# Optimization experiments

Measured on AMD Instinct MI355X. Metric: run time of the kernel, lower is better.

## Reference

```python
import jax, jax.numpy as jnp
import numpy as np

N = 50000     # nodes
E = 800000    # edges (avg degree 16)
DIN = 128     # in_size
DH = 256      # hidden_size
P = 100000    # pos/neg edge pairs


def _w(key, fan_in, shape):
    return jax.random.normal(key, shape, jnp.float32) * (1.0 / np.sqrt(fan_in))


def setup_inputs() -> dict:
    key = jax.random.key(0)
    ks = jax.random.split(key, 24)
    inp = {}
    inp['x'] = jax.random.normal(ks[0], (N, DIN), jnp.float32)
    inp['edge_src'] = jax.random.randint(ks[1], (E,), 0, N, dtype=jnp.int32)
    inp['edge_dst'] = jax.random.randint(ks[2], (E,), 0, N, dtype=jnp.int32)
    inp['pos_src'] = jax.random.randint(ks[3], (P,), 0, N, dtype=jnp.int32)
    inp['pos_dst'] = jax.random.randint(ks[4], (P,), 0, N, dtype=jnp.int32)
    inp['neg_src'] = jax.random.randint(ks[5], (P,), 0, N, dtype=jnp.int32)
    inp['neg_dst'] = jax.random.randint(ks[6], (P,), 0, N, dtype=jnp.int32)
    # SAGEConv layers: fc_self + fc_neigh + bias
    dims = [(DIN, DH), (DH, DH), (DH, DH)]
    for i, (di, do) in enumerate(dims):
        inp[f'Ws{i}'] = _w(ks[7 + 3 * i], di, (di, do))
        inp[f'Wn{i}'] = _w(ks[8 + 3 * i], di, (di, do))
        inp[f'b{i}'] = jnp.zeros((do,), jnp.float32)
    # predictor MLP: DH -> DH -> DH -> 1
    inp['Wp1'] = _w(ks[16], DH, (DH, DH)); inp['bp1'] = jnp.zeros((DH,), jnp.float32)
    inp['Wp2'] = _w(ks[17], DH, (DH, DH)); inp['bp2'] = jnp.zeros((DH,), jnp.float32)
    inp['Wp3'] = _w(ks[18], DH, (DH, 1)); inp['bp3'] = jnp.zeros((1,), jnp.float32)
    return inp


def _sage_layer(h, src, dst, Ws, Wn, b):
    # mean aggregation over incoming edges, then fc_self(h) + fc_neigh(agg) + b
    n = h.shape[0]
    msg = h[src]                                              # [E, d] gather
    deg = jax.ops.segment_sum(jnp.ones((src.shape[0],), h.dtype), dst, num_segments=n)
    agg = jax.ops.segment_sum(msg, dst, num_segments=n)
    agg = agg / jnp.maximum(deg, 1.0)[:, None]
    return h @ Ws + agg @ Wn + b


def reference(x, edge_src, edge_dst, pos_src, pos_dst, neg_src, neg_dst,
              Ws0, Wn0, b0, Ws1, Wn1, b1, Ws2, Wn2, b2,
              Wp1, bp1, Wp2, bp2, Wp3, bp3):
    h = x
    layers = [(Ws0, Wn0, b0), (Ws1, Wn1, b1), (Ws2, Wn2, b2)]
    for i, (Ws, Wn, bb) in enumerate(layers):
        h = _sage_layer(h, edge_src, edge_dst, Ws, Wn, bb)
        if i < len(layers) - 1:
            h = jax.nn.relu(h)

    def predictor(e):
        z = jax.nn.relu(e @ Wp1 + bp1)
        z = jax.nn.relu(z @ Wp2 + bp2)
        return z @ Wp3 + bp3

    hidden_pos = predictor(h[pos_src] * h[pos_dst])   # [P, 1]
    hidden_neg = predictor(h[neg_src] * h[neg_dst])   # [P, 1]
    return (hidden_pos, hidden_neg)
```

## Files before the change

### kernel.cpp

```cpp
#include <hip/hip_runtime.h>
#include <hip/hip_bf16.h>

#define CDIV(a, b) (((a) + (b) - 1) / (b))

typedef __attribute__((ext_vector_type(8))) __bf16 bf16x8;
typedef __attribute__((ext_vector_type(2))) __bf16 bf16x2;
typedef __attribute__((ext_vector_type(4))) float f32x4;

__device__ __forceinline__ float bf2f(unsigned short u) {
  union { unsigned int i; float f; } c; c.i = ((unsigned int)u) << 16; return c.f;
}
__device__ __forceinline__ unsigned short f2bf(float f) {
  union { float f; unsigned int i; } c; c.f = f;
  unsigned int r = c.i + 0x7fffu + ((c.i >> 16) & 1u);
  return (unsigned short)(r >> 16);
}
__device__ __forceinline__ unsigned int cvt2(float a, float b) {
  bf16x2 v; v[0] = (__bf16)a; v[1] = (__bf16)b;
  union { bf16x2 v; unsigned int u; } c; c.v = v; return c.u;
}
__device__ __forceinline__ unsigned short cvt1(float a) {
  __bf16 b = (__bf16)a;
  union { __bf16 b; unsigned short u; } c; c.b = b; return c.u;
}

__global__ void k_detect(const unsigned short* __restrict__ xq, int nsamp, int* __restrict__ flagp) {
  __shared__ float sm[256];
  int t = threadIdx.x;
  float mx = 0.f;
  for (int i = t; i < nsamp; i += 256) {
    float v = bf2f(xq[i]);
    if (!(v == v)) v = 1e30f;
    mx = fmaxf(mx, fabsf(v));
  }
  sm[t] = mx; __syncthreads();
  for (int o = 128; o > 0; o >>= 1) {
    if (t < o) sm[t] = fmaxf(sm[t], sm[t + o]);
    __syncthreads();
  }
  if (t == 0) *flagp = (sm[0] > 1e6f) ? 1 : 0;
}

__global__ void k_cvt7(const void* p0, const void* p1, const void* p2, const void* p3,
                       const void* p4, const void* p5, const void* p6,
                       float* d0, float* d1, float* d2, float* d3,
                       float* d4, float* d5, float* d6, const int* __restrict__ flagp) {
  int b = blockIdx.x, t = threadIdx.x;
  const void* s = 0; float* d = 0; int n = 256;
  switch (b) {
    case 0: s = p0; d = d0; break;
    case 1: s = p1; d = d1; break;
    case 2: s = p2; d = d2; break;
    case 3: s = p3; d = d3; break;
    case 4: s = p4; d = d4; break;
    case 5: s = p5; d = d5; break;
    default: s = p6; d = d6; n = 1; break;
  }
  if (t < n) d[t] = (*flagp) ? ((const float*)s)[t] : bf2f(((const unsigned short*)s)[t]);
}

__global__ void k_wh(const void* __restrict__ W, unsigned short* __restrict__ Bth,
                     int K, const int* __restrict__ flagp) {
  int i = blockIdx.x * 256 + threadIdx.x;
  if (i >= K * 256) return;
  int k = i >> 8, n = i & 255;
  float v = (*flagp) ? ((const float*)W)[i] : bf2f(((const unsigned short*)W)[i]);
  Bth[(size_t)n * K + k] = f2bf(v);
}

__global__ void k_xbf16(const void* __restrict__ x, unsigned short* __restrict__ Xb, int n,
                        const int* __restrict__ flagp) {
  int i = blockIdx.x * 256 + threadIdx.x;
  if (i >= n) return;
  float v = (*flagp) ? ((const float*)x)[i] : bf2f(((const unsigned short*)x)[i]);
  Xb[i] = f2bf(v);
}

__global__ void k_zero_i32(int* p, int n) {
  int i = blockIdx.x * 256 + threadIdx.x;
  if (i < n) p[i] = 0;
}

__global__ void k_deg(const int* __restrict__ dst, int* __restrict__ deg, int E) {
  int e = blockIdx.x * 256 + threadIdx.x;
  if (e < E) atomicAdd(&deg[dst[e]], 1);
}
__global__ void k_scan1(const int* __restrict__ in, int* __restrict__ out, int* __restrict__ bsums, int n) {
  __shared__ int sh[256];
  int t = threadIdx.x, i = blockIdx.x * 256 + t;
  int v = (i < n) ? in[i] : 0;
  sh[t] = v; __syncthreads();
  for (int o = 1; o < 256; o <<= 1) {
    int add = (t >= o) ? sh[t - o] : 0;
    __syncthreads();
    sh[t] += add;
    __syncthreads();
  }
  if (i < n) out[i] = sh[t] - v;
  if (t == 255) bsums[blockIdx.x] = sh[255];
}
__global__ void k_scan2(int* bsums, int nb) {
  __shared__ int sh[256];
  int t = threadIdx.x;
  int v = (t < nb) ? bsums[t] : 0;
  sh[t] = v; __syncthreads();
  for (int o = 1; o < 256; o <<= 1) {
    int add = (t >= o) ? sh[t - o] : 0;
    __syncthreads();
    sh[t] += add;
    __syncthreads();
  }
  if (t < nb) bsums[t] = sh[t] - v;
}
__global__ void k_scan3(int* offs, const int* bsums, int n, int etot) {
  int i = blockIdx.x * 256 + threadIdx.x;
  if (i < n) offs[i] += bsums[blockIdx.x];
  if (i == 0) offs[n] = etot;
}
__global__ void k_copy_i32(const int* __restrict__ a, int* __restrict__ b, int n) {
  int i = blockIdx.x * 256 + threadIdx.x;
  if (i < n) b[i] = a[i];
}
__global__ void k_fill(const int* __restrict__ dst, const int* __restrict__ src,
                       int* __restrict__ cursor, int* __restrict__ csr_src, int E) {
  int e = blockIdx.x * 256 + threadIdx.x;
  if (e >= E) return;
  int pos = atomicAdd(&cursor[dst[e]], 1);
  csr_src[pos] = src[e];
}
__global__ void k_sortw(const int* __restrict__ offs, int* __restrict__ csr, int n) {
  int w = threadIdx.x >> 6, lane = threadIdx.x & 63;
  int v = blockIdx.x * 4 + w;
  if (v >= n) return;
  int s = offs[v], e = offs[v + 1];
  int deg = e - s;
  if (deg <= 1) return;
  if (deg > 64) {
    if (lane == 0) {
      for (int i = s + 1; i < e; ++i) {
        int key = csr[i], j = i - 1;
        while (j >= s && csr[j] > key) { csr[j + 1] = csr[j]; --j; }
        csr[j + 1] = key;
      }
    }
    return;
  }
  int val = (lane < deg) ? csr[s + lane] : 0x7fffffff;
#pragma unroll
  for (int k = 2; k <= 64; k <<= 1) {
    bool dir = (lane & k) == 0;
#pragma unroll
    for (int j = k >> 1; j > 0; j >>= 1) {
      int p = __shfl_xor(val, j, 64);
      bool lower = (lane & j) == 0;
      val = (lower == dir) ? min(val, p) : max(val, p);
    }
  }
  if (lane < deg) csr[s + lane] = val;
}

__global__ void k_agg(const unsigned short* __restrict__ H, int Kd,
                      const int* __restrict__ offs, const int* __restrict__ csr,
                      unsigned short* __restrict__ Ab) {
  int w = threadIdx.x >> 6, lane = threadIdx.x & 63;
  int v = blockIdx.x * 4 + w;
  int s = offs[v], e = offs[v + 1];
  float inv = 1.f / fmaxf((float)(e - s), 1.f);
  if (Kd == 256) {
    int c4 = lane * 4;
    float a0 = 0.f, a1 = 0.f, a2 = 0.f, a3 = 0.f;
    int i = s;
    for (; i + 4 <= e; i += 4) {
      uint2 z0 = *(const uint2*)&H[(size_t)csr[i] * 256 + c4];
      uint2 z1 = *(const uint2*)&H[(size_t)csr[i + 1] * 256 + c4];
      uint2 z2 = *(const uint2*)&H[(size_t)csr[i + 2] * 256 + c4];
      uint2 z3 = *(const uint2*)&H[(size_t)csr[i + 3] * 256 + c4];
      a0 += bf2f((unsigned short)z0.x) + bf2f((unsigned short)z1.x)
          + bf2f((unsigned short)z2.x) + bf2f((unsigned short)z3.x);
      a1 += bf2f((unsigned short)(z0.x >> 16)) + bf2f((unsigned short)(z1.x >> 16))
          + bf2f((unsigned short)(z2.x >> 16)) + bf2f((unsigned short)(z3.x >> 16));
      a2 += bf2f((unsigned short)z0.y) + bf2f((unsigned short)z1.y)
          + bf2f((unsigned short)z2.y) + bf2f((unsigned short)z3.y);
      a3 += bf2f((unsigned short)(z0.y >> 16)) + bf2f((unsigned short)(z1.y >> 16))
          + bf2f((unsigned short)(z2.y >> 16)) + bf2f((unsigned short)(z3.y >> 16));
    }
    for (; i < e; ++i) {
      uint2 z0 = *(const uint2*)&H[(size_t)csr[i] * 256 + c4];
      a0 += bf2f((unsigned short)z0.x);
      a1 += bf2f((unsigned short)(z0.x >> 16));
      a2 += bf2f((unsigned short)z0.y);
      a3 += bf2f((unsigned short)(z0.y >> 16));
    }
    uint2 o;
    o.x = cvt2(a0 * inv, a1 * inv);
    o.y = cvt2(a2 * inv, a3 * inv);
    *(uint2*)&Ab[(size_t)v * 256 + c4] = o;
  } else {
    int c2 = lane * 2;
    float a0 = 0.f, a1 = 0.f;
    int i = s;
    for (; i + 4 <= e; i += 4) {
      unsigned int z0 = *(const unsigned int*)&H[(size_t)csr[i] * 128 + c2];
      unsigned int z1 = *(const unsigned int*)&H[(size_t)csr[i + 1] * 128 + c2];
      unsigned int z2 = *(const unsigned int*)&H[(size_t)csr[i + 2] * 128 + c2];
      unsigned int z3 = *(const unsigned int*)&H[(size_t)csr[i + 3] * 128 + c2];
      a0 += bf2f((unsigned short)z0) + bf2f((unsigned short)z1)
          + bf2f((unsigned short)z2) + bf2f((unsigned short)z3);
      a1 += bf2f((unsigned short)(z0 >> 16)) + bf2f((unsigned short)(z1 >> 16))
          + bf2f((unsigned short)(z2 >> 16)) + bf2f((unsigned short)(z3 >> 16));
    }
    for (; i < e; ++i) {
      unsigned int z0 = *(const unsigned int*)&H[(size_t)csr[i] * 128 + c2];
      a0 += bf2f((unsigned short)z0);
      a1 += bf2f((unsigned short)(z0 >> 16));
    }
    *(unsigned int*)&Ab[(size_t)v * 128 + c2] = cvt2(a0 * inv, a1 * inv);
  }
}

__global__ __launch_bounds__(256) void gemm_cat(
    const unsigned short* __restrict__ A1, const unsigned short* __restrict__ A2, int K,
    const unsigned short* __restrict__ B1h, const unsigned short* __restrict__ B2h,
    const float* __restrict__ bias, int relu, int M, unsigned short* __restrict__ O) {
  __shared__ unsigned short sAh[128 * 40], sBh[128 * 40];
  int t = threadIdx.x;
  int mt = blockIdx.x >> 1, nt = blockIdx.x & 1;
  int m0 = mt * 128;
  int n0 = nt * 128;
  int wid = t >> 6, lane = t & 63;
  int wr = (wid >> 1) * 64, wc = (wid & 1) * 64;
  int quad = lane >> 4, lrow = lane & 15;

  f32x4 acc[4][4];
  const f32x4 z4 = {0.f, 0.f, 0.f, 0.f};
#pragma unroll
  for (int i = 0; i < 4; ++i)
#pragma unroll
    for (int j = 0; j < 4; ++j) acc[i][j] = z4;

  int sr = t >> 2;
  int c8 = (t & 3) * 8;
  int ar0 = m0 + sr;      if (ar0 >= M) ar0 = M - 1;
  int ar1 = m0 + sr + 64; if (ar1 >= M) ar1 = M - 1;
  int br0 = n0 + sr, br1 = n0 + sr + 64;

  int kc = K >> 5;
  int nsteps = kc * 2;

  uint4 pfA0 = *(const uint4*)&A1[(size_t)ar0 * K + c8];
  uint4 pfA1 = *(const uint4*)&A1[(size_t)ar1 * K + c8];
  uint4 pfB0 = *(const uint4*)&B1h[(size_t)br0 * K + c8];
  uint4 pfB1 = *(const uint4*)&B1h[(size_t)br1 * K + c8];

  for (int s2 = 0; s2 < nsteps; ++s2) {
    *(uint4*)&sAh[sr * 40 + c8] = pfA0;
    *(uint4*)&sAh[(sr + 64) * 40 + c8] = pfA1;
    *(uint4*)&sBh[sr * 40 + c8] = pfB0;
    *(uint4*)&sBh[(sr + 64) * 40 + c8] = pfB1;
    int s1 = s2 + 1;
    if (s1 < nsteps) {
      const unsigned short* Ap = (s1 >= kc) ? A2 : A1;
      const unsigned short* Bp = (s1 >= kc) ? B2h : B1h;
      int k0 = ((s1 >= kc) ? (s1 - kc) : s1) * 32;
      pfA0 = *(const uint4*)&Ap[(size_t)ar0 * K + k0 + c8];
      pfA1 = *(const uint4*)&Ap[(size_t)ar1 * K + k0 + c8];
      pfB0 = *(const uint4*)&Bp[(size_t)br0 * K + k0 + c8];
      pfB1 = *(const uint4*)&Bp[(size_t)br1 * K + k0 + c8];
    }
    __syncthreads();
    bf16x8 ah[4], bh[4];
#pragma unroll
    for (int i = 0; i < 4; ++i) {
      ah[i] = *(const bf16x8*)&sAh[(wr + i * 16 + lrow) * 40 + quad * 8];
      bh[i] = *(const bf16x8*)&sBh[(wc + i * 16 + lrow) * 40 + quad * 8];
    }
#pragma unroll
    for (int i = 0; i < 4; ++i)
#pragma unroll
      for (int j = 0; j < 4; ++j)
        acc[i][j] = __builtin_amdgcn_mfma_f32_16x16x32_bf16(ah[i], bh[j], acc[i][j], 0, 0, 0);
    __syncthreads();
  }

#pragma unroll
  for (int j = 0; j < 4; ++j) {
    int gc = n0 + wc + j * 16 + lrow;
    float bv = bias[gc];
#pragma unroll
    for (int i = 0; i < 4; ++i) {
#pragma unroll
      for (int rr = 0; rr < 4; ++rr) {
        int gr = m0 + wr + i * 16 + quad * 4 + rr;
        if (gr < M) {
          float v = acc[i][j][rr] + bv;
          if (relu) v = fmaxf(v, 0.f);
          O[(size_t)gr * 256 + gc] = cvt1(v);
        }
      }
    }
  }
}

__global__ __launch_bounds__(256, 3) void gemm_pred_fused(
    const unsigned short* __restrict__ Hb,
    const int* __restrict__ ps, const int* __restrict__ pd,
    const int* __restrict__ ns, const int* __restrict__ nd,
    int nPos,
    const unsigned short* __restrict__ B1h, const float* __restrict__ bp1c,
    const unsigned short* __restrict__ B2h, const float* __restrict__ bp2c,
    const float* __restrict__ wp3, const float* __restrict__ bp3c,
    void* __restrict__ out, const int* __restrict__ flagp) {
  __shared__ __align__(16) unsigned short zT[64 * 264];
  __shared__ __align__(16) unsigned short sBh[256 * 40];
  int t = threadIdx.x;
  int m0 = blockIdx.x * 64;
  int wid = t >> 6, lane = t & 63;
  int wc = wid * 64;
  int quad = lane >> 4, lrow = lane & 15;

  int sr = t >> 2;
  int c8 = (t & 3) * 8;
  int c64 = (t & 3) * 64;

  int arow = m0 + sr;
  int s, d;
  if (arow < nPos) { s = ps[arow]; d = pd[arow]; }
  else             { s = ns[arow - nPos]; d = nd[arow - nPos]; }
  const unsigned short* Hs = &Hb[(size_t)s * 256];
  const unsigned short* Hd = &Hb[(size_t)d * 256];

#pragma unroll
  for (int u = 0; u < 8; ++u) {
    uint4 hs = *(const uint4*)(Hs + c64 + u * 8);
    uint4 hd = *(const uint4*)(Hd + c64 + u * 8);
    uint4 o;
    o.x = cvt2(bf2f((unsigned short)hs.x) * bf2f((unsigned short)hd.x),
               bf2f((unsigned short)(hs.x >> 16)) * bf2f((unsigned short)(hd.x >> 16)));
    o.y = cvt2(bf2f((unsigned short)hs.y) * bf2f((unsigned short)hd.y),
               bf2f((unsigned short)(hs.y >> 16)) * bf2f((unsigned short)(hd.y >> 16)));
    o.z = cvt2(bf2f((unsigned short)hs.z) * bf2f((unsigned short)hd.z),
               bf2f((unsigned short)(hs.z >> 16)) * bf2f((unsigned short)(hd.z >> 16)));
    o.w = cvt2(bf2f((unsigned short)hs.w) * bf2f((unsigned short)hd.w),
               bf2f((unsigned short)(hs.w >> 16)) * bf2f((unsigned short)(hd.w >> 16)));
    *(uint4*)&zT[sr * 264 + c64 + u * 8] = o;
  }

  f32x4 acc[4][4];
  const f32x4 z4 = {0.f, 0.f, 0.f, 0.f};
#pragma unroll
  for (int i = 0; i < 4; ++i)
#pragma unroll
    for (int j = 0; j < 4; ++j) acc[i][j] = z4;

  for (int k0 = 0; k0 < 256; k0 += 32) {
#pragma unroll
    for (int rep = 0; rep < 4; ++rep) {
      int r = sr + rep * 64;
      *(uint4*)&sBh[r * 40 + c8] = *(const uint4*)&B1h[(size_t)r * 256 + k0 + c8];
    }
    __syncthreads();
    bf16x8 ah[4], bh[4];
#pragma unroll
    for (int i = 0; i < 4; ++i) {
      ah[i] = *(const bf16x8*)&zT[(i * 16 + lrow) * 264 + k0 + quad * 8];
      bh[i] = *(const bf16x8*)&sBh[(wc + i * 16 + lrow) * 40 + quad * 8];
    }
    __builtin_amdgcn_s_setprio(1);
#pragma unroll
    for (int i = 0; i < 4; ++i)
#pragma unroll
      for (int j = 0; j < 4; ++j)
        acc[i][j] = __builtin_amdgcn_mfma_f32_16x16x32_bf16(ah[i], bh[j], acc[i][j], 0, 0, 0);
    __builtin_amdgcn_s_setprio(0);
    __syncthreads();
  }

#pragma unroll
  for (int j = 0; j < 4; ++j) {
    int gc = wc + j * 16 + lrow;
    float bv = bp1c[gc];
#pragma unroll
    for (int i = 0; i < 4; ++i) {
#pragma unroll
      for (int rr = 0; rr < 4; ++rr) {
        int rloc = i * 16 + quad * 4 + rr;
        float v = fmaxf(acc[i][j][rr] + bv, 0.f);
        zT[rloc * 264 + gc] = cvt1(v);
      }
    }
  }

#pragma unroll
  for (int i = 0; i < 4; ++i)
#pragma unroll
    for (int j = 0; j < 4; ++j) acc[i][j] = z4;

  for (int k0 = 0; k0 < 256; k0 += 32) {
#pragma unroll
    for (int rep = 0; rep < 4; ++rep) {
      int r = sr + rep * 64;
      *(uint4*)&sBh[r * 40 + c8] = *(const uint4*)&B2h[(size_t)r * 256 + k0 + c8];
    }
    __syncthreads();
    bf16x8 ah[4], bh[4];
#pragma unroll
    for (int i = 0; i < 4; ++i) {
      ah[i] = *(const bf16x8*)&zT[(i * 16 + lrow) * 264 + k0 + quad * 8];
      bh[i] = *(const bf16x8*)&sBh[(wc + i * 16 + lrow) * 40 + quad * 8];
    }
    __builtin_amdgcn_s_setprio(1);
#pragma unroll
    for (int i = 0; i < 4; ++i)
#pragma unroll
      for (int j = 0; j < 4; ++j)
        acc[i][j] = __builtin_amdgcn_mfma_f32_16x16x32_bf16(ah[i], bh[j], acc[i][j], 0, 0, 0);
    __builtin_amdgcn_s_setprio(0);
    __syncthreads();
  }

  float* part = (float*)sBh;
  int cid = wid * 16 + lrow;
#pragma unroll
  for (int i = 0; i < 4; ++i) {
#pragma unroll
    for (int rr = 0; rr < 4; ++rr) {
      int rloc = i * 16 + quad * 4 + rr;
      float sum = 0.f;
#pragma unroll
      for (int j = 0; j < 4; ++j) {
        int gc = wc + j * 16 + lrow;
        float v = fmaxf(acc[i][j][rr] + bp2c[gc], 0.f);
        sum += v * wp3[gc];
      }
      part[rloc * 65 + cid] = sum;
    }
  }
  __syncthreads();
  if (t < 64) {
    int gr = m0 + t;
    float ssum = 0.f;
#pragma unroll
    for (int c = 0; c < 64; ++c) ssum += part[t * 65 + c];
    ssum += bp3c[0];
    if (*flagp) ((float*)out)[gr] = ssum;
    else        ((unsigned short*)out)[gr] = f2bf(ssum);
  }
}

extern "C" void kernel_launch(void* const* d_in, const int* in_sizes, int n_in,
                              void* d_out, int out_size, void* d_ws, size_t ws_size,
                              hipStream_t stream) {
  const int N = 50000, E = 800000, P = 100000, DIN = 128, DH = 256;
  const int M2 = 2 * P;
  const void* x = d_in[0];
  const int* esrc = (const int*)d_in[1];
  const int* edst = (const int*)d_in[2];
  const int* psrc = (const int*)d_in[3];
  const int* pdst = (const int*)d_in[4];
  const int* nsrc = (const int*)d_in[5];
  const int* ndst = (const int*)d_in[6];
  const void* Ws0 = d_in[7];  const void* Wn0 = d_in[8];  const void* b0 = d_in[9];
  const void* Ws1 = d_in[10]; const void* Wn1 = d_in[11]; const void* b1 = d_in[12];
  const void* Ws2 = d_in[13]; const void* Wn2 = d_in[14]; const void* b2 = d_in[15];
  const void* Wp1 = d_in[16]; const void* bp1 = d_in[17];
  const void* Wp2 = d_in[18]; const void* bp2 = d_in[19];
  const void* Wp3 = d_in[20]; const void* bp3 = d_in[21];
  (void)in_sizes; (void)n_in; (void)out_size; (void)ws_size;

  const size_t NH = (size_t)N * DH;
  unsigned short* planeA = (unsigned short*)d_ws;
  unsigned short* Xb = planeA;
  char* reg1 = (char*)d_ws + NH * 2;
  unsigned short* AggB  = (unsigned short*)reg1;
  unsigned short* planeB = (unsigned short*)(reg1 + NH * 4);
  float* P0 = (float*)(reg1 + (size_t)M2 * 256 * 2);
  float* P1 = P0 + M2;
  unsigned short* W16 = (unsigned short*)(P1 + M2);
  unsigned short* ws0h = W16;
  unsigned short* wn0h = ws0h + 32768;
  unsigned short* ws1h = wn0h + 32768;
  unsigned short* wn1h = ws1h + 65536;
  unsigned short* ws2h = wn1h + 65536;
  unsigned short* wn2h = ws2h + 65536;
  unsigned short* wp1h = wn2h + 65536;
  unsigned short* wp2h = wp1h + 65536;
  float* FB = (float*)(wp2h + 65536);
  float* b0f  = FB;
  float* b1f  = b0f + 256;
  float* b2f  = b1f + 256;
  float* bp1f = b2f + 256;
  float* bp2f = bp1f + 256;
  float* wp3f = bp2f + 256;
  float* bp3f = wp3f + 256;
  int* deg   = (int*)(bp3f + 4);
  int* offs  = deg + N;
  int* cur   = offs + (N + 1);
  int* bsums = cur + N;
  int* csr   = bsums + 256;
  int* flagp = csr + E;

  k_detect<<<1, 256, 0, stream>>>((const unsigned short*)x, 8192, flagp);

  k_wh<<<CDIV(DIN * DH, 256), 256, 0, stream>>>(Ws0, ws0h, DIN, flagp);
  k_wh<<<CDIV(DIN * DH, 256), 256, 0, stream>>>(Wn0, wn0h, DIN, flagp);
  k_wh<<<CDIV(DH * DH, 256), 256, 0, stream>>>(Ws1, ws1h, DH, flagp);
  k_wh<<<CDIV(DH * DH, 256), 256, 0, stream>>>(Wn1, wn1h, DH, flagp);
  k_wh<<<CDIV(DH * DH, 256), 256, 0, stream>>>(Ws2, ws2h, DH, flagp);
  k_wh<<<CDIV(DH * DH, 256), 256, 0, stream>>>(Wn2, wn2h, DH, flagp);
  k_wh<<<CDIV(DH * DH, 256), 256, 0, stream>>>(Wp1, wp1h, DH, flagp);
  k_wh<<<CDIV(DH * DH, 256), 256, 0, stream>>>(Wp2, wp2h, DH, flagp);
  k_cvt7<<<7, 256, 0, stream>>>(b0, b1, b2, bp1, bp2, Wp3, bp3,
                                b0f, b1f, b2f, bp1f, bp2f, wp3f, bp3f, flagp);

  int nb = CDIV(N, 256);
  k_zero_i32<<<nb, 256, 0, stream>>>(deg, N);
  k_deg<<<CDIV(E, 256), 256, 0, stream>>>(edst, deg, E);
  k_scan1<<<nb, 256, 0, stream>>>(deg, offs, bsums, N);
  k_scan2<<<1, 256, 0, stream>>>(bsums, nb);
  k_scan3<<<nb, 256, 0, stream>>>(offs, bsums, N, E);
  k_copy_i32<<<nb, 256, 0, stream>>>(offs, cur, N);
  k_fill<<<CDIV(E, 256), 256, 0, stream>>>(edst, esrc, cur, csr, E);
  k_sortw<<<CDIV(N, 4), 256, 0, stream>>>(offs, csr, N);

  const int G_L = CDIV(N, 128) * 2;

  k_xbf16<<<CDIV(N * DIN, 256), 256, 0, stream>>>(x, Xb, N * DIN, flagp);
  k_agg<<<N / 4, 256, 0, stream>>>(Xb, DIN, offs, csr, AggB);
  gemm_cat<<<G_L, 256, 0, stream>>>(Xb, AggB, DIN, ws0h, wn0h, b0f, 1, N, planeB);

  k_agg<<<N / 4, 256, 0, stream>>>(planeB, DH, offs, csr, AggB);
  gemm_cat<<<G_L, 256, 0, stream>>>(planeB, AggB, DH, ws1h, wn1h, b1f, 1, N, planeA);

  k_agg<<<N / 4, 256, 0, stream>>>(planeA, DH, offs, csr, AggB);
  gemm_cat<<<G_L, 256, 0, stream>>>(planeA, AggB, DH, ws2h, wn2h, b2f, 0, N, planeB);

  gemm_pred_fused<<<M2 / 64, 256, 0, stream>>>(planeB, psrc, pdst, nsrc, ndst, P,
                                               wp1h, bp1f, wp2h, bp2f, wp3f, bp3f,
                                               d_out, flagp);
}
```

Baseline: 640.0 us.

## Swizzle predictor LDS layouts, merge weight-transpose launches into one kernel

```diff
diff --git a/kernel.cpp b/kernel.cpp
--- a/kernel.cpp
+++ b/kernel.cpp
@@ -59,13 +59,32 @@
   if (t < n) d[t] = (*flagp) ? ((const float*)s)[t] : bf2f(((const unsigned short*)s)[t]);
 }
 
-__global__ void k_wh(const void* __restrict__ W, unsigned short* __restrict__ Bth,
-                     int K, const int* __restrict__ flagp) {
-  int i = blockIdx.x * 256 + threadIdx.x;
-  if (i >= K * 256) return;
+__global__ void k_wh8(const void* s0, const void* s1, const void* s2, const void* s3,
+                      const void* s4, const void* s5, const void* s6, const void* s7,
+                      unsigned short* d0, unsigned short* d1, unsigned short* d2,
+                      unsigned short* d3, unsigned short* d4, unsigned short* d5,
+                      unsigned short* d6, unsigned short* d7,
+                      const int* __restrict__ flagp) {
+  int b = blockIdx.x;
+  const void* W; unsigned short* Bt; int K; int base;
+  if (b < 128)       { W = s0; Bt = d0; K = 128; base = 0; }
+  else if (b < 256)  { W = s1; Bt = d1; K = 128; base = 128; }
+  else {
+    int r = (b - 256) >> 8;
+    base = 256 + r * 256; K = 256;
+    switch (r) {
+      case 0:  W = s2; Bt = d2; break;
+      case 1:  W = s3; Bt = d3; break;
+      case 2:  W = s4; Bt = d4; break;
+      case 3:  W = s5; Bt = d5; break;
+      case 4:  W = s6; Bt = d6; break;
+      default: W = s7; Bt = d7; break;
+    }
+  }
+  int i = (b - base) * 256 + threadIdx.x;
   int k = i >> 8, n = i & 255;
   float v = (*flagp) ? ((const float*)W)[i] : bf2f(((const unsigned short*)W)[i]);
-  Bth[(size_t)n * K + k] = f2bf(v);
+  Bt[(size_t)n * K + k] = f2bf(v);
 }
 
 __global__ void k_xbf16(const void* __restrict__ x, unsigned short* __restrict__ Xb, int n,
@@ -311,7 +330,7 @@
     const float* __restrict__ wp3, const float* __restrict__ bp3c,
     void* __restrict__ out, const int* __restrict__ flagp) {
   __shared__ __align__(16) unsigned short zT[64 * 264];
-  __shared__ __align__(16) unsigned short sBh[256 * 40];
+  __shared__ __align__(16) unsigned short sBh[256 * 38];
   int t = threadIdx.x;
   int m0 = blockIdx.x * 64;
   int wid = t >> 6, lane = t & 63;
@@ -320,19 +339,19 @@
 
   int sr = t >> 2;
   int c8 = (t & 3) * 8;
-  int c64 = (t & 3) * 64;
+  int cq = t & 3;
 
   int arow = m0 + sr;
   int s, d;
   if (arow < nPos) { s = ps[arow]; d = pd[arow]; }
   else             { s = ns[arow - nPos]; d = nd[arow - nPos]; }
-  const unsigned short* Hs = &Hb[(size_t)s * 256];
-  const unsigned short* Hd = &Hb[(size_t)d * 256];
+  const unsigned short* Hs = &Hb[(size_t)s * 256 + cq * 64];
+  const unsigned short* Hd = &Hb[(size_t)d * 256 + cq * 64];
 
 #pragma unroll
   for (int u = 0; u < 8; ++u) {
-    uint4 hs = *(const uint4*)(Hs + c64 + u * 8);
-    uint4 hd = *(const uint4*)(Hd + c64 + u * 8);
+    uint4 hs = *(const uint4*)(Hs + u * 8);
+    uint4 hd = *(const uint4*)(Hd + u * 8);
     uint4 o;
     o.x = cvt2(bf2f((unsigned short)hs.x) * bf2f((unsigned short)hd.x),
                bf2f((unsigned short)(hs.x >> 16)) * bf2f((unsigned short)(hd.x >> 16)));
@@ -342,7 +361,7 @@
                bf2f((unsigned short)(hs.z >> 16)) * bf2f((unsigned short)(hd.z >> 16)));
     o.w = cvt2(bf2f((unsigned short)hs.w) * bf2f((unsigned short)hd.w),
                bf2f((unsigned short)(hs.w >> 16)) * bf2f((unsigned short)(hd.w >> 16)));
-    *(uint4*)&zT[sr * 264 + c64 + u * 8] = o;
+    *(uint4*)&zT[sr * 264 + cq * 64 + 8 * (u ^ cq)] = o;
   }
 
   f32x4 acc[4][4];
@@ -352,40 +371,44 @@
 #pragma unroll
     for (int j = 0; j < 4; ++j) acc[i][j] = z4;
 
-  for (int k0 = 0; k0 < 256; k0 += 32) {
+#pragma unroll
+  for (int ss = 0; ss < 8; ++ss) {
+    int k0 = ss * 32;
 #pragma unroll
     for (int rep = 0; rep < 4; ++rep) {
       int r = sr + rep * 64;
-      *(uint4*)&sBh[r * 40 + c8] = *(const uint4*)&B1h[(size_t)r * 256 + k0 + c8];
+      *(uint4*)&sBh[r * 38 + c8] = *(const uint4*)&B1h[(size_t)r * 256 + k0 + c8];
     }
     __syncthreads();
     bf16x8 ah[4], bh[4];
 #pragma unroll
     for (int i = 0; i < 4; ++i) {
-      ah[i] = *(const bf16x8*)&zT[(i * 16 + lrow) * 264 + k0 + quad * 8];
-      bh[i] = *(const bf16x8*)&sBh[(wc + i * 16 + lrow) * 40 + quad * 8];
-    }
-    __builtin_amdgcn_s_setprio(1);
+      ah[i] = *(const bf16x8*)&zT[(i * 16 + lrow) * 264 + k0 + 8 * (quad ^ (ss >> 1))];
+      bh[i] = *(const bf16x8*)&sBh[(wc + i * 16 + lrow) * 38 + quad * 8];
+    }
 #pragma unroll
     for (int i = 0; i < 4; ++i)
 #pragma unroll
       for (int j = 0; j < 4; ++j)
         acc[i][j] = __builtin_amdgcn_mfma_f32_16x16x32_bf16(ah[i], bh[j], acc[i][j], 0, 0, 0);
-    __builtin_amdgcn_s_setprio(0);
     __syncthreads();
   }
 
 #pragma unroll
   for (int j = 0; j < 4; ++j) {
-    int gc = wc + j * 16 + lrow;
-    float bv = bp1c[gc];
+    int col = wc + j * 16 + lrow;
+    float bv = bp1c[col];
 #pragma unroll
     for (int i = 0; i < 4; ++i) {
 #pragma unroll
       for (int rr = 0; rr < 4; ++rr) {
         int rloc = i * 16 + quad * 4 + rr;
         float v = fmaxf(acc[i][j][rr] + bv, 0.f);
-        zT[rloc * 264 + gc] = cvt1(v);
+        float vn = __shfl_xor(v, 1, 64);
+        if (!(lrow & 1)) {
+          int c2 = col ^ (wid << 3);
+          *(unsigned int*)&zT[rloc * 264 + c2] = cvt2(v, vn);
+        }
       }
     }
   }
@@ -395,26 +418,28 @@
 #pragma unroll
     for (int j = 0; j < 4; ++j) acc[i][j] = z4;
 
-  for (int k0 = 0; k0 < 256; k0 += 32) {
+  __syncthreads();
+
+#pragma unroll
+  for (int ss = 0; ss < 8; ++ss) {
+    int k0 = ss * 32;
 #pragma unroll
     for (int rep = 0; rep < 4; ++rep) {
       int r = sr + rep * 64;
-      *(uint4*)&sBh[r * 40 + c8] = *(const uint4*)&B2h[(size_t)r * 256 + k0 + c8];
+      *(uint4*)&sBh[r * 38 + c8] = *(const uint4*)&B2h[(size_t)r * 256 + k0 + c8];
     }
     __syncthreads();
     bf16x8 ah[4], bh[4];
 #pragma unroll
     for (int i = 0; i < 4; ++i) {
-      ah[i] = *(const bf16x8*)&zT[(i * 16 + lrow) * 264 + k0 + quad * 8];
-      bh[i] = *(const bf16x8*)&sBh[(wc + i * 16 + lrow) * 40 + quad * 8];
-    }
-    __builtin_amdgcn_s_setprio(1);
+      ah[i] = *(const bf16x8*)&zT[(i * 16 + lrow) * 264 + k0 + 8 * (quad ^ (ss >> 1))];
+      bh[i] = *(const bf16x8*)&sBh[(wc + i * 16 + lrow) * 38 + quad * 8];
+    }
 #pragma unroll
     for (int i = 0; i < 4; ++i)
 #pragma unroll
       for (int j = 0; j < 4; ++j)
         acc[i][j] = __builtin_amdgcn_mfma_f32_16x16x32_bf16(ah[i], bh[j], acc[i][j], 0, 0, 0);
-    __builtin_amdgcn_s_setprio(0);
     __syncthreads();
   }
 
@@ -501,14 +526,9 @@
 
   k_detect<<<1, 256, 0, stream>>>((const unsigned short*)x, 8192, flagp);
 
-  k_wh<<<CDIV(DIN * DH, 256), 256, 0, stream>>>(Ws0, ws0h, DIN, flagp);
-  k_wh<<<CDIV(DIN * DH, 256), 256, 0, stream>>>(Wn0, wn0h, DIN, flagp);
-  k_wh<<<CDIV(DH * DH, 256), 256, 0, stream>>>(Ws1, ws1h, DH, flagp);
-  k_wh<<<CDIV(DH * DH, 256), 256, 0, stream>>>(Wn1, wn1h, DH, flagp);
-  k_wh<<<CDIV(DH * DH, 256), 256, 0, stream>>>(Ws2, ws2h, DH, flagp);
-  k_wh<<<CDIV(DH * DH, 256), 256, 0, stream>>>(Wn2, wn2h, DH, flagp);
-  k_wh<<<CDIV(DH * DH, 256), 256, 0, stream>>>(Wp1, wp1h, DH, flagp);
-  k_wh<<<CDIV(DH * DH, 256), 256, 0, stream>>>(Wp2, wp2h, DH, flagp);
+  k_wh8<<<1792, 256, 0, stream>>>(Ws0, Wn0, Ws1, Wn1, Ws2, Wn2, Wp1, Wp2,
+                                  ws0h, wn0h, ws1h, wn1h, ws2h, wn2h, wp1h, wp2h,
+                                  flagp);
   k_cvt7<<<7, 256, 0, stream>>>(b0, b1, b2, bp1, bp2, Wp3, bp3,
                                 b0f, b1f, b2f, bp1f, bp2f, wp3f, bp3f, flagp);
 
```

Result: faster. 619.6 us (-3.2%).
